# Kernel optimization log

Measured on AMD Instinct MI355X. Metric: run time of the kernel, lower is better.

The kernel has to match this reference:

```python
import jax, jax.numpy as jnp
import numpy as np

N_NODES = 100000
N_EDGES = 1000000
N_GRAPHS = 5000
H = 64
F_IN = 14  # QM9 num_features (11) + pos (3)
BN_EPS = 1e-5


def setup_inputs() -> dict:
    key = jax.random.key(0)
    ks = jax.random.split(key, 16)

    def w(k, shape, fan_in):
        return (jax.random.normal(k, shape, jnp.float32) / np.sqrt(fan_in)).astype(jnp.float32)

    inp = {
        "x": jax.random.normal(ks[0], (N_NODES, 11), jnp.float32),
        "pos": jax.random.normal(ks[1], (N_NODES, 3), jnp.float32),
        "edge_index": jax.random.randint(ks[2], (2, N_EDGES), 0, N_NODES, dtype=jnp.int32),
        "batch": jnp.sort(jax.random.randint(ks[3], (N_NODES,), 0, N_GRAPHS, dtype=jnp.int32)),
    }
    dims = [F_IN, H, H]
    i = 4
    for l, din in enumerate(dims, 1):
        inp[f"w{l}a"] = w(ks[i], (din, H), din); i += 1
        inp[f"b{l}a"] = jnp.zeros((H,), jnp.float32)
        inp[f"g{l}"] = jnp.ones((H,), jnp.float32)   # BatchNorm gamma
        inp[f"be{l}"] = jnp.zeros((H,), jnp.float32)  # BatchNorm beta
        inp[f"w{l}b"] = w(ks[i], (H, H), H); i += 1
        inp[f"b{l}b"] = jnp.zeros((H,), jnp.float32)
    inp["wl1"] = w(ks[i], (3 * H, H), 3 * H); i += 1
    inp["bl1"] = jnp.zeros((H,), jnp.float32)
    inp["wl2"] = w(ks[i], (H, 1), H)
    inp["bl2"] = jnp.zeros((1,), jnp.float32)
    return inp


def _gin_layer(x, src, dst, w1, b1, g, be, w2, b2):
    # GINConv (eps=0): h = MLP(x + sum_{j in N(i)} x_j)
    agg = jax.ops.segment_sum(x[src], dst, num_segments=x.shape[0])
    h = (x + agg) @ w1 + b1
    # BatchNorm1d in training mode: batch stats over node dim (biased var)
    mu = jnp.mean(h, axis=0)
    var = jnp.mean((h - mu) ** 2, axis=0)
    h = jax.nn.relu(g * (h - mu) * jax.lax.rsqrt(var + BN_EPS) + be)
    return jax.nn.relu(h @ w2 + b2)


def _mean_pool(x, batch):
    s = jax.ops.segment_sum(x, batch, num_segments=N_GRAPHS)
    c = jax.ops.segment_sum(jnp.ones((x.shape[0], 1), x.dtype), batch, num_segments=N_GRAPHS)
    return s / jnp.maximum(c, 1.0)


def reference(x, pos, edge_index, batch,
              w1a, b1a, g1, be1, w1b, b1b,
              w2a, b2a, g2, be2, w2b, b2b,
              w3a, b3a, g3, be3, w3b, b3b,
              wl1, bl1, wl2, bl2):
    src, dst = edge_index[0], edge_index[1]
    h0 = jnp.concatenate([x, pos], axis=1)                 # [N, 14]
    x1 = _gin_layer(h0, src, dst, w1a, b1a, g1, be1, w1b, b1b)
    x2 = _gin_layer(x1, src, dst, w2a, b2a, g2, be2, w2b, b2b)
    x3 = _gin_layer(x2, src, dst, w3a, b3a, g3, be3, w3b, b3b)
    p = jnp.concatenate([_mean_pool(x1, batch), _mean_pool(x2, batch), _mean_pool(x3, batch)], axis=1)  # [G, 192]
    h = jax.nn.relu(p @ wl1 + bl1)
    return h @ wl2 + bl2                                   # [G, 1]
```

## Files before the change

kernel.cpp:

```cpp
#include <hip/hip_runtime.h>
#include <hip/hip_bf16.h>

#define BN_EPS 1e-5f
#define LDP 132
#define LDS_BF 72
#define BSH 9
#define EPB 4096

typedef short bf16x8 __attribute__((ext_vector_type(8)));
typedef float f32x4 __attribute__((ext_vector_type(4)));

__device__ __forceinline__ float loadf(const void* p, long long i, unsigned bf) {
    if (bf) return __bfloat162float(((const __hip_bfloat16*)p)[i]);
    return ((const float*)p)[i];
}
__device__ __forceinline__ float b2f(unsigned short u) {
    return __uint_as_float(((unsigned)u) << 16);
}
__device__ __forceinline__ unsigned short f2b(float f) {
    __hip_bfloat16 h = __float2bfloat16(f);
    return *(unsigned short*)&h;
}
__device__ __forceinline__ float blo(unsigned u) { return __uint_as_float(u << 16); }
__device__ __forceinline__ float bhi(unsigned u) { return __uint_as_float(u & 0xffff0000u); }
__device__ __forceinline__ unsigned bfflag(const unsigned* g1w) {
    return (*g1w == 0x3F803F80u) ? 1u : 0u;
}

struct Srcs { const void* p[22]; };

__global__ void k_convert(Srcs s, const unsigned* g1w, float* dst, unsigned short* wbt) {
    unsigned bf = bfflag(g1w);
    int t = blockIdx.x;
    if (t < 22) {
        const int sizes[22] = {896,64,64,64,4096,64,  4096,64,64,64,4096,64,
                               4096,64,64,64,4096,64, 12288,64,64,1};
        const int offs[22]  = {0,896,960,1024,1088,5184, 5248,9344,9408,9472,9536,13632,
                               13696,17792,17856,17920,17984,22080, 22144,34432,34496,34560};
        const void* src = s.p[t];
        float* d = dst + offs[t];
        int n = sizes[t];
        for (int i = threadIdx.x; i < n; i += blockDim.x) d[i] = loadf(src, i, bf);
    } else {
        const int widx[5] = {4, 6, 10, 12, 16};
        const void* src = s.p[widx[t - 22]];
        unsigned short* dw = wbt + (t - 22) * 4096;
        for (int i = threadIdx.x; i < 4096; i += blockDim.x) {
            int n = i >> 6, k = i & 63;
            dw[n * 64 + k] = f2b(loadf(src, (long long)k * 64 + n, bf));
        }
    }
}

__global__ __launch_bounds__(256) void k_build(const void* x, const void* pos, const int* batch,
                        const unsigned* g1w, unsigned short* h0b, float* cnt, int N) {
    int i = blockIdx.x * blockDim.x + threadIdx.x;
    if (i >= N) return;
    unsigned bf = bfflag(g1w);
    unsigned short v[16];
    #pragma unroll
    for (int k = 0; k < 11; k++) v[k] = f2b(loadf(x, (long long)i * 11 + k, bf));
    #pragma unroll
    for (int k = 0; k < 3; k++) v[11 + k] = f2b(loadf(pos, (long long)i * 3 + k, bf));
    v[14] = 0; v[15] = 0;
    #pragma unroll
    for (int k = 0; k < 4; k++)
        *(ushort4*)&h0b[(long long)i * 16 + k * 4] = make_ushort4(v[4*k], v[4*k+1], v[4*k+2], v[4*k+3]);
    atomicAdd(&cnt[batch[i]], 1.0f);
}

__global__ __launch_bounds__(256) void k_bhist(const int* __restrict__ ei, int* __restrict__ bcnt,
                                               int E, int NCH, int NBK) {
    __shared__ int h[1024];
    int c = blockIdx.x, t = threadIdx.x;
    for (int i = t; i < NBK; i += 256) h[i] = 0;
    __syncthreads();
    int base = c * EPB;
    for (int i = t; i < EPB; i += 256) {
        int e = base + i;
        if (e < E) atomicAdd(&h[ei[E + e] >> BSH], 1);
    }
    __syncthreads();
    for (int i = t; i < NBK; i += 256) bcnt[i * NCH + c] = h[i];
}

__global__ __launch_bounds__(256) void k_scan_partial(const int* __restrict__ src, int* partial, int M) {
    __shared__ int sr[4];
    int b = blockIdx.x, t = threadIdx.x;
    int base = b * 1024;
    int s = 0;
    #pragma unroll
    for (int k = 0; k < 4; k++) {
        int i = base + k * 256 + t;
        if (i < M) s += src[i];
    }
    #pragma unroll
    for (int off = 32; off; off >>= 1) s += __shfl_down(s, off);
    if ((t & 63) == 0) sr[t >> 6] = s;
    __syncthreads();
    if (t == 0) partial[b] = sr[0] + sr[1] + sr[2] + sr[3];
}

__global__ __launch_bounds__(1024) void k_scan_chunks(const int* partial, int* chunkoff, int nchunks) {
    __shared__ int sp[1024];
    int t = threadIdx.x;
    sp[t] = (t < nchunks) ? partial[t] : 0;
    __syncthreads();
    for (int off = 1; off < 1024; off <<= 1) {
        int v = (t >= off) ? sp[t - off] : 0;
        __syncthreads();
        sp[t] += v;
        __syncthreads();
    }
    if (t < nchunks) chunkoff[t] = (t == 0) ? 0 : sp[t - 1];
}

__global__ __launch_bounds__(256) void k_scan_final(const int* __restrict__ src, const int* chunkoff,
                                                    int* __restrict__ out, int M) {
    __shared__ int sp[256];
    int b = blockIdx.x, t = threadIdx.x;
    int base = b * 1024 + t * 4;
    int v0 = 0, v1 = 0, v2 = 0, v3 = 0;
    if (base + 0 < M) v0 = src[base + 0];
    if (base + 1 < M) v1 = src[base + 1];
    if (base + 2 < M) v2 = src[base + 2];
    if (base + 3 < M) v3 = src[base + 3];
    int s = v0 + v1 + v2 + v3;
    sp[t] = s;
    __syncthreads();
    for (int off = 1; off < 256; off <<= 1) {
        int v = (t >= off) ? sp[t - off] : 0;
        __syncthreads();
        sp[t] += v;
        __syncthreads();
    }
    int run = chunkoff[b] + sp[t] - s;
    if (base + 0 < M) { out[base + 0] = run; run += v0; }
    if (base + 1 < M) { out[base + 1] = run; run += v1; }
    if (base + 2 < M) { out[base + 2] = run; run += v2; }
    if (base + 3 < M) { out[base + 3] = run; }
}

__global__ __launch_bounds__(256) void k_place(const int* __restrict__ ei, const int* __restrict__ boff,
                                               unsigned* __restrict__ ebuf, int E, int NCH, int NBK) {
    __shared__ int cur[1024];
    int c = blockIdx.x, t = threadIdx.x;
    for (int i = t; i < NBK; i += 256) cur[i] = boff[i * NCH + c];
    __syncthreads();
    int base = c * EPB;
    for (int i = t; i < EPB; i += 256) {
        int e = base + i;
        if (e < E) {
            int s = ei[e], d = ei[E + e];
            int pos = atomicAdd(&cur[d >> BSH], 1);
            ebuf[pos] = ((unsigned)(d & 511) << 23) | (unsigned)s;
        }
    }
}

__global__ __launch_bounds__(256) void k_bucket_fill(const unsigned* __restrict__ ebuf, const int* __restrict__ boff,
                                                     int* __restrict__ roff, int* __restrict__ csr,
                                                     int N, int E, int NCH, int NBK) {
    __shared__ int cnt[512];
    __shared__ int exc[512];
    __shared__ int curb[512];
    __shared__ int sp[256];
    int b = blockIdx.x, t = threadIdx.x;
    int d0 = b << BSH;
    int dpb = N - d0; if (dpb > 512) dpb = 512;
    int segS = boff[b * NCH];
    int segE = (b + 1 < NBK) ? boff[(b + 1) * NCH] : E;
    cnt[t] = 0; cnt[t + 256] = 0;
    __syncthreads();
    for (int k = segS + t; k < segE; k += 256) atomicAdd(&cnt[ebuf[k] >> 23], 1);
    __syncthreads();
    int a0 = cnt[2 * t], a1 = cnt[2 * t + 1];
    sp[t] = a0 + a1;
    __syncthreads();
    for (int off = 1; off < 256; off <<= 1) {
        int v = (t >= off) ? sp[t - off] : 0;
        __syncthreads();
        sp[t] += v;
        __syncthreads();
    }
    int pre = (t == 0) ? 0 : sp[t - 1];
    exc[2 * t] = pre; exc[2 * t + 1] = pre + a0;
    curb[2 * t] = pre; curb[2 * t + 1] = pre + a0;
    __syncthreads();
    for (int i = t; i < dpb; i += 256) roff[d0 + i] = segS + exc[i];
    if (b == NBK - 1 && t == 0) roff[N] = E;
    for (int k = segS + t; k < segE; k += 256) {
        unsigned p = ebuf[k];
        int lp = atomicAdd(&curb[p >> 23], 1);
        csr[segS + lp] = (int)(p & 0x7FFFFFu);
    }
}

__global__ __launch_bounds__(256) void k_gather14b(const int* __restrict__ roff, const int* __restrict__ csr,
                                                   const unsigned short* __restrict__ h0b,
                                                   unsigned short* __restrict__ aggb, int N) {
    int q = threadIdx.x & 7, nn = threadIdx.x >> 3;
    int node = blockIdx.x * 32 + nn;
    if (node >= N) return;
    const unsigned* h0u = (const unsigned*)h0b;
    unsigned su = h0u[(long long)node * 8 + q];
    float a0 = blo(su), a1 = bhi(su);
    float b0 = 0.f, b1 = 0.f, c0 = 0.f, c1 = 0.f, d0 = 0.f, d1 = 0.f;
    int e0 = roff[node], e1 = roff[node + 1];
    int k = e0;
    for (; k + 3 < e1; k += 4) {
        unsigned u0 = h0u[(long long)csr[k] * 8 + q];
        unsigned u1 = h0u[(long long)csr[k + 1] * 8 + q];
        unsigned u2 = h0u[(long long)csr[k + 2] * 8 + q];
        unsigned u3 = h0u[(long long)csr[k + 3] * 8 + q];
        a0 += blo(u0); a1 += bhi(u0);
        b0 += blo(u1); b1 += bhi(u1);
        c0 += blo(u2); c1 += bhi(u2);
        d0 += blo(u3); d1 += bhi(u3);
    }
    for (; k < e1; k++) {
        unsigned u0 = h0u[(long long)csr[k] * 8 + q];
        a0 += blo(u0); a1 += bhi(u0);
    }
    a0 += b0 + c0 + d0; a1 += b1 + c1 + d1;
    unsigned outw = (unsigned)f2b(a0) | ((unsigned)f2b(a1) << 16);
    ((unsigned*)aggb)[(long long)node * 8 + q] = outw;
}

__global__ __launch_bounds__(256) void k_mm_bn14b(const unsigned short* __restrict__ aggb,
        const float* __restrict__ W, const float* __restrict__ bias, unsigned short* __restrict__ Hb,
        float* bnsum, float* bnsumsq, int N) {
    __shared__ float sA[14 * LDP];
    __shared__ float sW[14 * 64];
    __shared__ float sRs[4 * 64];
    __shared__ float sRq[4 * 64];
    int tid = threadIdx.x;
    int row0 = blockIdx.x * 128;
    int rows = N - row0; if (rows > 128) rows = 128;
    for (int i = tid; i < 14 * 64; i += 256) sW[i] = W[i];
    const unsigned* au = (const unsigned*)aggb;
    #pragma unroll
    for (int it = 0; it < 4; it++) {
        int idx = tid + it * 256;
        int r = idx >> 3, q = idx & 7;
        unsigned u = (r < rows) ? au[(long long)(row0 + r) * 8 + q] : 0u;
        if (2 * q < 14)     sA[(2 * q) * LDP + r] = blo(u);
        if (2 * q + 1 < 14) sA[(2 * q + 1) * LDP + r] = bhi(u);
    }
    __syncthreads();
    int tx = tid & 15, ty = tid >> 4;
    float4 bj = *(const float4*)&bias[tx * 4];
    float acc[8][4];
    #pragma unroll
    for (int i = 0; i < 8; i++) { acc[i][0] = bj.x; acc[i][1] = bj.y; acc[i][2] = bj.z; acc[i][3] = bj.w; }
    #pragma unroll
    for (int k = 0; k < 14; k++) {
        const float4 a0 = *(const float4*)&sA[k * LDP + ty * 8];
        const float4 a1 = *(const float4*)&sA[k * LDP + ty * 8 + 4];
        const float4 w  = *(const float4*)&sW[k * 64 + tx * 4];
        const float av[8] = {a0.x, a0.y, a0.z, a0.w, a1.x, a1.y, a1.z, a1.w};
        #pragma unroll
        for (int i = 0; i < 8; i++) {
            acc[i][0] += av[i] * w.x; acc[i][1] += av[i] * w.y;
            acc[i][2] += av[i] * w.z; acc[i][3] += av[i] * w.w;
        }
    }
    float cs[4] = {0.f, 0.f, 0.f, 0.f}, cq[4] = {0.f, 0.f, 0.f, 0.f};
    #pragma unroll
    for (int i = 0; i < 8; i++) {
        int r = ty * 8 + i;
        if (r < rows) {
            int gr = row0 + r;
            ushort4 hv;
            hv.x = f2b(acc[i][0]); hv.y = f2b(acc[i][1]);
            hv.z = f2b(acc[i][2]); hv.w = f2b(acc[i][3]);
            *(ushort4*)&Hb[(long long)gr * 64 + tx * 4] = hv;
            #pragma unroll
            for (int d = 0; d < 4; d++) { cs[d] += acc[i][d]; cq[d] += acc[i][d] * acc[i][d]; }
        }
    }
    #pragma unroll
    for (int d = 0; d < 4; d++) {
        cs[d] += __shfl_xor(cs[d], 16); cs[d] += __shfl_xor(cs[d], 32);
        cq[d] += __shfl_xor(cq[d], 16); cq[d] += __shfl_xor(cq[d], 32);
    }
    int wid = tid >> 6, lane = tid & 63;
    if (lane < 16) {
        #pragma unroll
        for (int d = 0; d < 4; d++) {
            sRs[wid * 64 + lane * 4 + d] = cs[d];
            sRq[wid * 64 + lane * 4 + d] = cq[d];
        }
    }
    __syncthreads();
    if (tid < 64) atomicAdd(&bnsum[tid], sRs[tid] + sRs[64 + tid] + sRs[128 + tid] + sRs[192 + tid]);
    else if (tid < 128) {
        int j = tid - 64;
        atomicAdd(&bnsumsq[j], sRq[j] + sRq[64 + j] + sRq[128 + j] + sRq[192 + j]);
    }
}

__global__ __launch_bounds__(256) void k_gather64(const int* __restrict__ roff, const int* __restrict__ csr,
                                                  const unsigned short* __restrict__ xinb,
                                                  unsigned short* __restrict__ aggb, int N) {
    int g = threadIdx.x >> 4, q = threadIdx.x & 15;
    int node = blockIdx.x * 16 + g;
    if (node >= N) return;
    const ushort4* xr = (const ushort4*)xinb;
    ushort4 u = xr[(long long)node * 16 + q];
    float4 a0 = make_float4(b2f(u.x), b2f(u.y), b2f(u.z), b2f(u.w));
    float4 a1 = make_float4(0.f, 0.f, 0.f, 0.f);
    float4 a2 = make_float4(0.f, 0.f, 0.f, 0.f);
    float4 a3 = make_float4(0.f, 0.f, 0.f, 0.f);
    int e0 = roff[node], e1 = roff[node + 1];
    int k = e0;
    for (; k + 3 < e1; k += 4) {
        int s0 = csr[k], s1 = csr[k + 1], s2 = csr[k + 2], s3 = csr[k + 3];
        ushort4 v0 = xr[(long long)s0 * 16 + q];
        ushort4 v1 = xr[(long long)s1 * 16 + q];
        ushort4 v2 = xr[(long long)s2 * 16 + q];
        ushort4 v3 = xr[(long long)s3 * 16 + q];
        a0.x += b2f(v0.x); a0.y += b2f(v0.y); a0.z += b2f(v0.z); a0.w += b2f(v0.w);
        a1.x += b2f(v1.x); a1.y += b2f(v1.y); a1.z += b2f(v1.z); a1.w += b2f(v1.w);
        a2.x += b2f(v2.x); a2.y += b2f(v2.y); a2.z += b2f(v2.z); a2.w += b2f(v2.w);
        a3.x += b2f(v3.x); a3.y += b2f(v3.y); a3.z += b2f(v3.z); a3.w += b2f(v3.w);
    }
    for (; k < e1; k++) {
        ushort4 v0 = xr[(long long)csr[k] * 16 + q];
        a0.x += b2f(v0.x); a0.y += b2f(v0.y); a0.z += b2f(v0.z); a0.w += b2f(v0.w);
    }
    a0.x += a1.x + a2.x + a3.x;
    a0.y += a1.y + a2.y + a3.y;
    a0.z += a1.z + a2.z + a3.z;
    a0.w += a1.w + a2.w + a3.w;
    ushort4 o;
    o.x = f2b(a0.x); o.y = f2b(a0.y); o.z = f2b(a0.z); o.w = f2b(a0.w);
    *(ushort4*)&aggb[(long long)node * 64 + q * 4] = o;
}

__global__ __launch_bounds__(256) void k_mm_bn64(const unsigned short* __restrict__ Sb,
        const unsigned short* __restrict__ Wt,
        const float* __restrict__ bias, unsigned short* __restrict__ Hb,
        float* bnsum, float* bnsumsq, int N) {
    __shared__ unsigned short sS[128 * LDS_BF];
    __shared__ unsigned short sWt[64 * LDS_BF];
    __shared__ float sRs[4 * 64];
    __shared__ float sRq[4 * 64];
    int tid = threadIdx.x;
    int row0 = blockIdx.x * 128;
    int rows = N - row0; if (rows > 128) rows = 128;
    #pragma unroll
    for (int it = 0; it < 8; it++) {
        int idx = tid + it * 256;
        int r = idx >> 4, q = idx & 15;
        ushort4 v = make_ushort4(0, 0, 0, 0);
        if (r < rows) v = *(const ushort4*)&Sb[(long long)(row0 + r) * 64 + (q << 2)];
        *(ushort4*)&sS[r * LDS_BF + q * 4] = v;
    }
    #pragma unroll
    for (int it = 0; it < 4; it++) {
        int i = tid + it * 256;
        ushort4 v = ((const ushort4*)Wt)[i];
        int n = i >> 4, k4 = (i & 15) << 2;
        *(ushort4*)&sWt[n * LDS_BF + k4] = v;
    }
    __syncthreads();
    int w = tid >> 6, lane = tid & 63;
    int half = lane >> 4, m = lane & 15;
    f32x4 acc[2][4];
    #pragma unroll
    for (int rt = 0; rt < 2; rt++)
        #pragma unroll
        for (int ct = 0; ct < 4; ct++) acc[rt][ct] = (f32x4){0.f, 0.f, 0.f, 0.f};
    #pragma unroll
    for (int km = 0; km < 2; km++) {
        bf16x8 a0 = *(const bf16x8*)&sS[(w * 32 + m) * LDS_BF + km * 32 + half * 8];
        bf16x8 a1 = *(const bf16x8*)&sS[(w * 32 + 16 + m) * LDS_BF + km * 32 + half * 8];
        #pragma unroll
        for (int ct = 0; ct < 4; ct++) {
            bf16x8 b = *(const bf16x8*)&sWt[(ct * 16 + m) * LDS_BF + km * 32 + half * 8];
            acc[0][ct] = __builtin_amdgcn_mfma_f32_16x16x32_bf16(a0, b, acc[0][ct], 0, 0, 0);
            acc[1][ct] = __builtin_amdgcn_mfma_f32_16x16x32_bf16(a1, b, acc[1][ct], 0, 0, 0);
        }
    }
    float cs[4] = {0.f, 0.f, 0.f, 0.f}, cq[4] = {0.f, 0.f, 0.f, 0.f};
    #pragma unroll
    for (int ct = 0; ct < 4; ct++) {
        float bj = bias[ct * 16 + m];
        #pragma unroll
        for (int rt = 0; rt < 2; rt++) {
            #pragma unroll
            for (int r = 0; r < 4; r++) {
                int lr = w * 32 + rt * 16 + half * 4 + r;
                if (lr < rows) {
                    float v = acc[rt][ct][r] + bj;
                    Hb[(long long)(row0 + lr) * 64 + ct * 16 + m] = f2b(v);
                    cs[ct] += v; cq[ct] += v * v;
                }
            }
        }
    }
    #pragma unroll
    for (int d = 0; d < 4; d++) {
        cs[d] += __shfl_xor(cs[d], 16); cs[d] += __shfl_xor(cs[d], 32);
        cq[d] += __shfl_xor(cq[d], 16); cq[d] += __shfl_xor(cq[d], 32);
    }
    if (lane < 16) {
        #pragma unroll
        for (int ct = 0; ct < 4; ct++) {
            sRs[w * 64 + ct * 16 + lane] = cs[ct];
            sRq[w * 64 + ct * 16 + lane] = cq[ct];
        }
    }
    __syncthreads();
    if (tid < 64) atomicAdd(&bnsum[tid], sRs[tid] + sRs[64 + tid] + sRs[128 + tid] + sRs[192 + tid]);
    else if (tid < 128) {
        int j = tid - 64;
        atomicAdd(&bnsumsq[j], sRq[j] + sRq[64 + j] + sRq[128 + j] + sRq[192 + j]);
    }
}

__global__ __launch_bounds__(256) void k_bn_mm2_rt(const unsigned short* __restrict__ Hb, const float* __restrict__ g,
        const float* __restrict__ be, const unsigned short* __restrict__ Wt, const float* __restrict__ b2,
        const float* bnsum, const float* bnsumsq, const int* __restrict__ batch,
        unsigned short* __restrict__ xout, float* pool, int N, float invN, int loff) {
    __shared__ unsigned short sS[128 * LDS_BF];
    __shared__ unsigned short sWt[64 * LDS_BF];
    __shared__ float sSc[64];
    __shared__ float sSh[64];
    int tid = threadIdx.x;
    int row0 = blockIdx.x * 128;
    int rows = N - row0; if (rows > 128) rows = 128;
    if (tid < 64) {
        float mu = bnsum[tid] * invN;
        float var = bnsumsq[tid] * invN - mu * mu;
        float sc = g[tid] * rsqrtf(var + BN_EPS);
        sSc[tid] = sc; sSh[tid] = be[tid] - sc * mu;
    }
    #pragma unroll
    for (int it = 0; it < 4; it++) {
        int i = tid + it * 256;
        ushort4 v = ((const ushort4*)Wt)[i];
        int n = i >> 4, k4 = (i & 15) << 2;
        *(ushort4*)&sWt[n * LDS_BF + k4] = v;
    }
    __syncthreads();
    #pragma unroll
    for (int it = 0; it < 8; it++) {
        int idx = tid + it * 256;
        int r = idx >> 4, q = idx & 15;
        ushort4 o = make_ushort4(0, 0, 0, 0);
        if (r < rows) {
            ushort4 u = *(const ushort4*)&Hb[(long long)(row0 + r) * 64 + (q << 2)];
            o.x = f2b(fmaxf(sSc[q*4+0] * b2f(u.x) + sSh[q*4+0], 0.f));
            o.y = f2b(fmaxf(sSc[q*4+1] * b2f(u.y) + sSh[q*4+1], 0.f));
            o.z = f2b(fmaxf(sSc[q*4+2] * b2f(u.z) + sSh[q*4+2], 0.f));
            o.w = f2b(fmaxf(sSc[q*4+3] * b2f(u.w) + sSh[q*4+3], 0.f));
        }
        *(ushort4*)&sS[r * LDS_BF + q * 4] = o;
    }
    __syncthreads();
    int w = tid >> 6, lane = tid & 63;
    int half = lane >> 4, m = lane & 15;
    f32x4 acc[2][4];
    #pragma unroll
    for (int rt = 0; rt < 2; rt++)
        #pragma unroll
        for (int ct = 0; ct < 4; ct++) acc[rt][ct] = (f32x4){0.f, 0.f, 0.f, 0.f};
    #pragma unroll
    for (int km = 0; km < 2; km++) {
        bf16x8 a0 = *(const bf16x8*)&sS[(w * 32 + m) * LDS_BF + km * 32 + half * 8];
        bf16x8 a1 = *(const bf16x8*)&sS[(w * 32 + 16 + m) * LDS_BF + km * 32 + half * 8];
        #pragma unroll
        for (int ct = 0; ct < 4; ct++) {
            bf16x8 b = *(const bf16x8*)&sWt[(ct * 16 + m) * LDS_BF + km * 32 + half * 8];
            acc[0][ct] = __builtin_amdgcn_mfma_f32_16x16x32_bf16(a0, b, acc[0][ct], 0, 0, 0);
            acc[1][ct] = __builtin_amdgcn_mfma_f32_16x16x32_bf16(a1, b, acc[1][ct], 0, 0, 0);
        }
    }
    float b2j[4];
    #pragma unroll
    for (int ct = 0; ct < 4; ct++) b2j[ct] = b2[ct * 16 + m];
    int prevg = -1;
    float p[4] = {0.f, 0.f, 0.f, 0.f};
    #pragma unroll
    for (int rt = 0; rt < 2; rt++) {
        #pragma unroll
        for (int r = 0; r < 4; r++) {
            int lr = w * 32 + rt * 16 + half * 4 + r;
            if (lr < rows) {
                int gr = row0 + lr;
                float o[4];
                #pragma unroll
                for (int ct = 0; ct < 4; ct++) {
                    o[ct] = fmaxf(acc[rt][ct][r] + b2j[ct], 0.f);
                    if (xout) xout[(long long)gr * 64 + ct * 16 + m] = f2b(o[ct]);
                }
                int gid = batch[gr];
                if (gid != prevg) {
                    if (prevg >= 0) {
                        float* pp = &pool[(long long)prevg * 192 + loff + m];
                        atomicAdd(pp + 0,  p[0]); atomicAdd(pp + 16, p[1]);
                        atomicAdd(pp + 32, p[2]); atomicAdd(pp + 48, p[3]);
                    }
                    prevg = gid;
                    p[0] = o[0]; p[1] = o[1]; p[2] = o[2]; p[3] = o[3];
                } else {
                    p[0] += o[0]; p[1] += o[1]; p[2] += o[2]; p[3] += o[3];
                }
            }
        }
    }
    if (prevg >= 0) {
        float* pp = &pool[(long long)prevg * 192 + loff + m];
        atomicAdd(pp + 0,  p[0]); atomicAdd(pp + 16, p[1]);
        atomicAdd(pp + 32, p[2]); atomicAdd(pp + 48, p[3]);
    }
}

__global__ __launch_bounds__(64) void k_head(const float* pool, const float* cnt,
                        const float* wl1, const float* bl1, const float* wl2, const float* bl2,
                        const unsigned* g1w, void* out, int G) {
    int gb = blockIdx.x; int j = threadIdx.x;
    if (gb >= G) return;
    __shared__ float sP[192];
    float c = fmaxf(cnt[gb], 1.0f);
    float inv = 1.0f / c;
    for (int k = j; k < 192; k += 64) sP[k] = pool[(long long)gb * 192 + k] * inv;
    __syncthreads();
    float acc = bl1[j];
    for (int k = 0; k < 192; k++) acc += sP[k] * wl1[k * 64 + j];
    float v = fmaxf(acc, 0.f) * wl2[j];
    #pragma unroll
    for (int off = 32; off; off >>= 1) v += __shfl_down(v, off);
    if (j == 0) {
        float res = v + bl2[0];
        if (bfflag(g1w)) ((__hip_bfloat16*)out)[gb] = __float2bfloat16(res);
        else             ((float*)out)[gb] = res;
    }
}

extern "C" void kernel_launch(void* const* d_in, const int* in_sizes, int n_in,
                              void* d_out, int out_size, void* d_ws, size_t ws_size,
                              hipStream_t stream) {
    const void* x   = d_in[0];
    const void* pos = d_in[1];
    const int* ei    = (const int*)d_in[2];
    const int* batch = (const int*)d_in[3];
    const unsigned* g1w = (const unsigned*)d_in[6];
    const int N = in_sizes[3];
    const int E = in_sizes[2] / 2;
    const int G = out_size;

    float* ws = (float*)d_ws;
    float* P = ws + 16;
    float* w1a = P + 0;     float* b1a = P + 896;   float* g1 = P + 960;   float* be1 = P + 1024;
    float* b1b = P + 5184;
    float* b2a = P + 9344;  float* g2 = P + 9408;  float* be2 = P + 9472;
    float* b2b = P + 13632;
    float* b3a = P + 17792; float* g3 = P + 17856; float* be3 = P + 17920;
    float* b3b = P + 22080;
    float* wl1 = P + 22144; float* bl1 = P + 34432; float* wl2 = P + 34496; float* bl2 = P + 34560;

    long long off = 16 + 34592;
    unsigned short* wbt = (unsigned short*)(ws + off);  off += 10240;
    float* h0r  = ws + off;                 off += (long long)N * 14;
    float* aggr = ws + off;                 off += (long long)N * 64;
    float* Hbuf = ws + off;                 off += (long long)N * 64;
    float* curf = ws + off;                 off += (long long)N * 64;
    float* pool = ws + off;                 off += (long long)G * 192;
    float* cnt  = ws + off;                 off += G;
    float* bn   = ws + off;                 off += 384;
    int*   roff = (int*)(ws + off);
    int* csr = roff + (N + 1);

    unsigned short* h0b  = (unsigned short*)h0r;
    unsigned short* aggh = (unsigned short*)aggr;
    unsigned short* curh = (unsigned short*)curf;
    unsigned short* Hh   = (unsigned short*)Hbuf;
    unsigned short* w1bT = wbt + 0 * 4096;
    unsigned short* w2aT = wbt + 1 * 4096;
    unsigned short* w2bT = wbt + 2 * 4096;
    unsigned short* w3aT = wbt + 3 * 4096;
    unsigned short* w3bT = wbt + 4 * 4096;

    const int NBK = (N + 511) >> BSH;
    const int NCH = (E + EPB - 1) / EPB;
    const int M = NBK * NCH;
    int* bcnt     = csr + E;
    int* boff     = bcnt + M;
    int* partial  = boff + M;
    int* chunkoff = partial + 1024;
    unsigned* ebuf = (unsigned*)Hbuf;

    hipMemsetAsync(pool, 0, ((size_t)G * 192 + (size_t)G + 384) * sizeof(float), stream);

    Srcs s;
    for (int i = 0; i < 22; i++) s.p[i] = d_in[4 + i];
    k_convert<<<27, 256, 0, stream>>>(s, g1w, P, wbt);

    int nb = (N + 255) / 256;
    k_build<<<nb, 256, 0, stream>>>(x, pos, batch, g1w, h0b, cnt, N);

    k_bhist<<<NCH, 256, 0, stream>>>(ei, bcnt, E, NCH, NBK);
    int nchS = (M + 1023) / 1024;
    k_scan_partial<<<nchS, 256, 0, stream>>>(bcnt, partial, M);
    k_scan_chunks<<<1, 1024, 0, stream>>>(partial, chunkoff, nchS);
    k_scan_final<<<nchS, 256, 0, stream>>>(bcnt, chunkoff, boff, M);
    k_place<<<NCH, 256, 0, stream>>>(ei, boff, ebuf, E, NCH, NBK);
    k_bucket_fill<<<NBK, 256, 0, stream>>>(ebuf, boff, roff, csr, N, E, NCH, NBK);

    int rtBlocks = (N + 127) / 128;
    int gBlocks = (N + 15) / 16;
    int g14Blocks = (N + 31) / 32;
    float invN = 1.0f / (float)N;
    float* bn1 = bn;
    float* bn2 = bn + 128;
    float* bn3 = bn + 256;

    k_gather14b<<<g14Blocks, 256, 0, stream>>>(roff, csr, h0b, aggh, N);
    k_mm_bn14b<<<rtBlocks, 256, 0, stream>>>(aggh, w1a, b1a, Hh, bn1, bn1 + 64, N);
    k_bn_mm2_rt<<<rtBlocks, 256, 0, stream>>>(Hh, g1, be1, w1bT, b1b, bn1, bn1 + 64, batch,
                                              curh, pool, N, invN, 0);
    k_gather64<<<gBlocks, 256, 0, stream>>>(roff, csr, curh, aggh, N);
    k_mm_bn64<<<rtBlocks, 256, 0, stream>>>(aggh, w2aT, b2a, Hh, bn2, bn2 + 64, N);
    k_bn_mm2_rt<<<rtBlocks, 256, 0, stream>>>(Hh, g2, be2, w2bT, b2b, bn2, bn2 + 64, batch,
                                              curh, pool, N, invN, 64);
    k_gather64<<<gBlocks, 256, 0, stream>>>(roff, csr, curh, aggh, N);
    k_mm_bn64<<<rtBlocks, 256, 0, stream>>>(aggh, w3aT, b3a, Hh, bn3, bn3 + 64, N);
    k_bn_mm2_rt<<<rtBlocks, 256, 0, stream>>>(Hh, g3, be3, w3bT, b3b, bn3, bn3 + 64, batch,
                                              nullptr, pool, N, invN, 128);

    k_head<<<G, 64, 0, stream>>>(pool, cnt, wl1, bl1, wl2, bl2, g1w, d_out, G);
}
```

Measured before the change: 349.0 us.

## Merge prep kernels and collapse three-pass bucket scan into one kernel

Fuses the weight-conversion and node-feature build kernels into one launch. The histogram kernel now also accumulates per-bucket totals with global atomics, which lets a single scan kernel (one block per bucket) produce all bucket-chunk offsets. That replaces the three-kernel partial/chunk/final scan. The aim is fewer kernel launches and less serialization in CSR construction, at the cost of global atomics. It also assumes NBK ≤ 256, which holds for N=100000 (196 buckets).

```diff
diff --git a/kernel.cpp b/kernel.cpp
--- a/kernel.cpp
+++ b/kernel.cpp
@@ -29,7 +29,9 @@
 
 struct Srcs { const void* p[22]; };
 
-__global__ void k_convert(Srcs s, const unsigned* g1w, float* dst, unsigned short* wbt) {
+__global__ __launch_bounds__(256) void k_prep(Srcs s, const unsigned* g1w, float* dst, unsigned short* wbt,
+                                              const void* x, const void* pos, const int* batch,
+                                              unsigned short* h0b, float* cnt, int N) {
     unsigned bf = bfflag(g1w);
     int t = blockIdx.x;
     if (t < 22) {
@@ -41,7 +43,7 @@
         float* d = dst + offs[t];
         int n = sizes[t];
         for (int i = threadIdx.x; i < n; i += blockDim.x) d[i] = loadf(src, i, bf);
-    } else {
+    } else if (t < 27) {
         const int widx[5] = {4, 6, 10, 12, 16};
         const void* src = s.p[widx[t - 22]];
         unsigned short* dw = wbt + (t - 22) * 4096;
@@ -49,28 +51,24 @@
             int n = i >> 6, k = i & 63;
             dw[n * 64 + k] = f2b(loadf(src, (long long)k * 64 + n, bf));
         }
-    }
-}
-
-__global__ __launch_bounds__(256) void k_build(const void* x, const void* pos, const int* batch,
-                        const unsigned* g1w, unsigned short* h0b, float* cnt, int N) {
-    int i = blockIdx.x * blockDim.x + threadIdx.x;
-    if (i >= N) return;
-    unsigned bf = bfflag(g1w);
-    unsigned short v[16];
-    #pragma unroll
-    for (int k = 0; k < 11; k++) v[k] = f2b(loadf(x, (long long)i * 11 + k, bf));
-    #pragma unroll
-    for (int k = 0; k < 3; k++) v[11 + k] = f2b(loadf(pos, (long long)i * 3 + k, bf));
-    v[14] = 0; v[15] = 0;
-    #pragma unroll
-    for (int k = 0; k < 4; k++)
-        *(ushort4*)&h0b[(long long)i * 16 + k * 4] = make_ushort4(v[4*k], v[4*k+1], v[4*k+2], v[4*k+3]);
-    atomicAdd(&cnt[batch[i]], 1.0f);
+    } else {
+        int i = (t - 27) * 256 + threadIdx.x;
+        if (i >= N) return;
+        unsigned short v[16];
+        #pragma unroll
+        for (int k = 0; k < 11; k++) v[k] = f2b(loadf(x, (long long)i * 11 + k, bf));
+        #pragma unroll
+        for (int k = 0; k < 3; k++) v[11 + k] = f2b(loadf(pos, (long long)i * 3 + k, bf));
+        v[14] = 0; v[15] = 0;
+        #pragma unroll
+        for (int k = 0; k < 4; k++)
+            *(ushort4*)&h0b[(long long)i * 16 + k * 4] = make_ushort4(v[4*k], v[4*k+1], v[4*k+2], v[4*k+3]);
+        atomicAdd(&cnt[batch[i]], 1.0f);
+    }
 }
 
 __global__ __launch_bounds__(256) void k_bhist(const int* __restrict__ ei, int* __restrict__ bcnt,
-                                               int E, int NCH, int NBK) {
+                                               int* __restrict__ bktot, int E, int NCH, int NBK) {
     __shared__ int h[1024];
     int c = blockIdx.x, t = threadIdx.x;
     for (int i = t; i < NBK; i += 256) h[i] = 0;
@@ -81,64 +79,44 @@
         if (e < E) atomicAdd(&h[ei[E + e] >> BSH], 1);
     }
     __syncthreads();
-    for (int i = t; i < NBK; i += 256) bcnt[i * NCH + c] = h[i];
-}
-
-__global__ __launch_bounds__(256) void k_scan_partial(const int* __restrict__ src, int* partial, int M) {
-    __shared__ int sr[4];
+    for (int i = t; i < NBK; i += 256) {
+        bcnt[i * NCH + c] = h[i];
+        if (h[i]) atomicAdd(&bktot[i], h[i]);
+    }
+}
+
+__global__ __launch_bounds__(256) void k_scan_all(const int* __restrict__ bcnt, const int* __restrict__ bktot,
+                                                  int* __restrict__ boff, int NCH, int NBK) {
+    __shared__ int sp[256];
+    __shared__ int sS;
     int b = blockIdx.x, t = threadIdx.x;
-    int base = b * 1024;
-    int s = 0;
-    #pragma unroll
-    for (int k = 0; k < 4; k++) {
-        int i = base + k * 256 + t;
-        if (i < M) s += src[i];
-    }
-    #pragma unroll
-    for (int off = 32; off; off >>= 1) s += __shfl_down(s, off);
-    if ((t & 63) == 0) sr[t >> 6] = s;
-    __syncthreads();
-    if (t == 0) partial[b] = sr[0] + sr[1] + sr[2] + sr[3];
-}
-
-__global__ __launch_bounds__(1024) void k_scan_chunks(const int* partial, int* chunkoff, int nchunks) {
-    __shared__ int sp[1024];
-    int t = threadIdx.x;
-    sp[t] = (t < nchunks) ? partial[t] : 0;
-    __syncthreads();
-    for (int off = 1; off < 1024; off <<= 1) {
-        int v = (t >= off) ? sp[t - off] : 0;
+    int v = (t < NBK) ? bktot[t] : 0;
+    sp[t] = v;
+    __syncthreads();
+    for (int off = 1; off < 256; off <<= 1) {
+        int u = (t >= off) ? sp[t - off] : 0;
         __syncthreads();
-        sp[t] += v;
+        sp[t] += u;
         __syncthreads();
     }
-    if (t < nchunks) chunkoff[t] = (t == 0) ? 0 : sp[t - 1];
-}
-
-__global__ __launch_bounds__(256) void k_scan_final(const int* __restrict__ src, const int* chunkoff,
-                                                    int* __restrict__ out, int M) {
-    __shared__ int sp[256];
-    int b = blockIdx.x, t = threadIdx.x;
-    int base = b * 1024 + t * 4;
-    int v0 = 0, v1 = 0, v2 = 0, v3 = 0;
-    if (base + 0 < M) v0 = src[base + 0];
-    if (base + 1 < M) v1 = src[base + 1];
-    if (base + 2 < M) v2 = src[base + 2];
-    if (base + 3 < M) v3 = src[base + 3];
-    int s = v0 + v1 + v2 + v3;
-    sp[t] = s;
-    __syncthreads();
-    for (int off = 1; off < 256; off <<= 1) {
-        int v = (t >= off) ? sp[t - off] : 0;
+    if (t == 0) sS = (b == 0) ? 0 : sp[b - 1];
+    __syncthreads();
+    int running = sS;
+    for (int base = 0; base < NCH; base += 256) {
+        int c = base + t;
+        int val = (c < NCH) ? bcnt[b * NCH + c] : 0;
         __syncthreads();
-        sp[t] += v;
+        sp[t] = val;
         __syncthreads();
-    }
-    int run = chunkoff[b] + sp[t] - s;
-    if (base + 0 < M) { out[base + 0] = run; run += v0; }
-    if (base + 1 < M) { out[base + 1] = run; run += v1; }
-    if (base + 2 < M) { out[base + 2] = run; run += v2; }
-    if (base + 3 < M) { out[base + 3] = run; }
+        for (int off = 1; off < 256; off <<= 1) {
+            int u = (t >= off) ? sp[t - off] : 0;
+            __syncthreads();
+            sp[t] += u;
+            __syncthreads();
+        }
+        if (c < NCH) boff[b * NCH + c] = running + sp[t] - val;
+        running += sp[255];
+    }
 }
 
 __global__ __launch_bounds__(256) void k_place(const int* __restrict__ ei, const int* __restrict__ boff,
@@ -571,6 +549,7 @@
     float* pool = ws + off;                 off += (long long)G * 192;
     float* cnt  = ws + off;                 off += G;
     float* bn   = ws + off;                 off += 384;
+    int* bktot  = (int*)(ws + off);         off += 256;
     int*   roff = (int*)(ws + off);
     int* csr = roff + (N + 1);
 
@@ -589,24 +568,17 @@
     const int M = NBK * NCH;
     int* bcnt     = csr + E;
     int* boff     = bcnt + M;
-    int* partial  = boff + M;
-    int* chunkoff = partial + 1024;
     unsigned* ebuf = (unsigned*)Hbuf;
 
-    hipMemsetAsync(pool, 0, ((size_t)G * 192 + (size_t)G + 384) * sizeof(float), stream);
+    hipMemsetAsync(pool, 0, ((size_t)G * 192 + (size_t)G + 384 + 256) * sizeof(float), stream);
 
     Srcs s;
     for (int i = 0; i < 22; i++) s.p[i] = d_in[4 + i];
-    k_convert<<<27, 256, 0, stream>>>(s, g1w, P, wbt);
-
     int nb = (N + 255) / 256;
-    k_build<<<nb, 256, 0, stream>>>(x, pos, batch, g1w, h0b, cnt, N);
-
-    k_bhist<<<NCH, 256, 0, stream>>>(ei, bcnt, E, NCH, NBK);
-    int nchS = (M + 1023) / 1024;
-    k_scan_partial<<<nchS, 256, 0, stream>>>(bcnt, partial, M);
-    k_scan_chunks<<<1, 1024, 0, stream>>>(partial, chunkoff, nchS);
-    k_scan_final<<<nchS, 256, 0, stream>>>(bcnt, chunkoff, boff, M);
+    k_prep<<<27 + nb, 256, 0, stream>>>(s, g1w, P, wbt, x, pos, batch, h0b, cnt, N);
+
+    k_bhist<<<NCH, 256, 0, stream>>>(ei, bcnt, bktot, E, NCH, NBK);
+    k_scan_all<<<NBK, 256, 0, stream>>>(bcnt, bktot, boff, NCH, NBK);
     k_place<<<NCH, 256, 0, stream>>>(ei, boff, ebuf, E, NCH, NBK);
     k_bucket_fill<<<NBK, 256, 0, stream>>>(ebuf, boff, roff, csr, N, E, NCH, NBK);
 
```

Measured after the change: 342.0 us. 1.02x faster.
